# Optimization experiments

Measured on AMD Instinct MI355X. Metric: run time of the kernel, lower is better.

The kernel has to match this reference:

```python
import jax, jax.numpy as jnp
import numpy as np

N_TIME = 512          # n_time_nodes
LATENT = 32           # latent_dim
HIDDEN = 64           # hidden_dim
N_MODES = 8           # r_fourier_modes
X_A0 = 0.3            # initial stoichiometry (anode)
CSANMAX = 28700.0     # max concentration scale
BASE_LOGIT = float(np.log(X_A0 / (1.0 - X_A0)))  # logit_from_fraction(x_a0)
FEAT_DIM = 1 + 2 * N_MODES   # [rho, cos(k*pi*rho), sin(k*pi*rho)]
IN_DIM = LATENT + FEAT_DIM
N_POINTS = 2_000_000


def setup_inputs() -> dict:
    key = jax.random.key(0)
    ks = jax.random.split(key, 8)
    time_idx = jax.random.randint(ks[0], (N_POINTS,), 0, N_TIME)
    rho = jax.random.uniform(ks[1], (N_POINTS,), dtype=jnp.float32)
    # trainable latent code per nonzero time node
    emb = jax.random.normal(ks[2], (N_TIME - 1, LATENT), dtype=jnp.float32) * 0.02
    # decoder_a: Linear(IN,HID)+SiLU, Linear(HID,HID)+SiLU, Linear(HID,1)
    W0 = jax.random.normal(ks[3], (IN_DIM, HIDDEN), dtype=jnp.float32) / np.sqrt(IN_DIM)
    b0 = jnp.zeros((HIDDEN,), jnp.float32)
    W1 = jax.random.normal(ks[4], (HIDDEN, HIDDEN), dtype=jnp.float32) / np.sqrt(HIDDEN)
    b1 = jnp.zeros((HIDDEN,), jnp.float32)
    Wout = jax.random.normal(ks[5], (HIDDEN, 1), dtype=jnp.float32) * 0.1
    bout = jnp.zeros((1,), jnp.float32)
    return {"time_idx": time_idx, "rho": rho, "emb": emb,
            "W0": W0, "b0": b0, "W1": W1, "b1": b1, "Wout": Wout, "bout": bout}


def _radius_features(rho):
    # [N] -> [N, 1 + 2*N_MODES]
    k = jnp.arange(1, N_MODES + 1, dtype=rho.dtype)
    ang = jnp.pi * rho[:, None] * k[None, :]
    return jnp.concatenate([rho[:, None], jnp.cos(ang), jnp.sin(ang)], axis=1)


def reference(time_idx, rho, emb, W0, b0, W1, b1, Wout, bout):
    # predicated version of the torch masked scatter: compute everywhere,
    # select initial-condition value where time_idx == 0
    idx = jnp.clip(time_idx - 1, 0, N_TIME - 2)       # safe gather index
    e = emb[idx]                                       # [N, LATENT]
    feat = _radius_features(rho)                       # [N, FEAT_DIM]
    h = jnp.concatenate([e, feat], axis=1)             # [N, IN_DIM]
    h = jax.nn.silu(h @ W0 + b0)
    h = jax.nn.silu(h @ W1 + b1)
    raw = (h @ Wout + bout)[:, 0]                      # [N]
    theta = jax.nn.sigmoid(raw + BASE_LOGIT)
    return jnp.where(time_idx == 0, X_A0 * CSANMAX, theta * CSANMAX)
```

## Files before the change

kernel.cpp:

```cpp
#include <hip/hip_runtime.h>
#include <stdint.h>


typedef _Float16 half8  __attribute__((ext_vector_type(8)));
typedef _Float16 half4v __attribute__((ext_vector_type(4)));
typedef _Float16 half2v __attribute__((ext_vector_type(2)));
typedef float f32x4 __attribute__((ext_vector_type(4)));

#define LOG2E 1.44269504088896340736f
#define BASE_LOGIT -0.84729786038720367f
#define CSANMAX 28700.0f
#define IC_VAL 8610.0f

__device__ __forceinline__ float fast_exp2(float x) { return __builtin_amdgcn_exp2f(x); }
__device__ __forceinline__ float fast_rcp(float x)  { return __builtin_amdgcn_rcpf(x); }
__device__ __forceinline__ float sigf(float x)  { return fast_rcp(1.0f + fast_exp2(-LOG2E * x)); }
__device__ __forceinline__ void silu2(float x0, float x1, float& y0, float& y1) {
  const float d0 = 1.0f + fast_exp2(-LOG2E * x0);
  const float d1 = 1.0f + fast_exp2(-LOG2E * x1);
  const float r  = fast_rcp(d0 * d1);
  y0 = x0 * d1 * r;
  y1 = x1 * d0 * r;
}
__device__ __forceinline__ half2v pkh(float a, float b) {
  return __builtin_bit_cast(half2v, __builtin_amdgcn_cvt_pkrtz(a, b));
}

union H8 { half8 v8; half2v v2[4]; };
union H4 { half4v v4; half2v v2[2]; };

template <int CTRL>
__device__ __forceinline__ float dpp_radd(float x) {
  int yi = __builtin_amdgcn_update_dpp(0, __builtin_bit_cast(int, x), CTRL, 0xF, 0xF, false);
  return x + __builtin_bit_cast(float, yi);
}
__device__ __forceinline__ float row_sum16(float x) {
  x = dpp_radd<0xB1>(x);
  x = dpp_radd<0x4E>(x);
  x = dpp_radd<0x141>(x);
  x = dpp_radd<0x140>(x);
  return x;
}

__global__ __launch_bounds__(256) void mlp_kernel(
    const int* __restrict__ tix, const float* __restrict__ rho,
    const float* __restrict__ emb, const float* __restrict__ W0,
    const float* __restrict__ b0, const float* __restrict__ W1,
    const float* __restrict__ b1, const float* __restrict__ Wout,
    const float* __restrict__ bout, float* __restrict__ out, int ngroups)
{
  __shared__ __align__(16) _Float16 Wlds0[2][4][64][8];
  __shared__ __align__(16) _Float16 Wlds1[2][4][64][8];
  __shared__ __align__(16) _Float16 ldsH[4][16][72];

  const int tid  = threadIdx.x;
  const int wid  = tid >> 6;
  const int lane = tid & 63;
  const int m    = lane & 15;
  const int q    = lane >> 4;

  _Float16 (*Hb)[72] = ldsH[wid];

  if (wid == 0) {
#pragma unroll
    for (int t = 0; t < 4; ++t) {
#pragma unroll
      for (int s = 0; s < 2; ++s) {
        half8 f0, f1;
#pragma unroll
        for (int j = 0; j < 8; ++j) {
          const int k = s * 32 + q * 8 + j;
          const int n = t * 16 + m;
          float v0;
          if (k < 32) {
            v0 = W0[k * 64 + n];
          } else {
            const int kn = k - 32;
            v0 = (kn < 16) ? W0[(33 + kn) * 64 + n]
               : (kn == 16) ? W0[32 * 64 + n]
               : (kn == 17) ? b0[n] : 0.0f;
          }
          f0[j] = (_Float16)v0;
          f1[j] = (_Float16)W1[k * 64 + n];
        }
        *(half8*)&Wlds0[s][t][lane][0] = f0;
        *(half8*)&Wlds1[s][t][lane][0] = f1;
      }
    }
  }

  float b1n[4], woutm[4];
#pragma unroll
  for (int t = 0; t < 4; ++t) {
    b1n[t]   = b1[t * 16 + m];
    woutm[t] = Wout[t * 16 + m];
  }
  const float boutBL = bout[0] + BASE_LOGIT;

  __syncthreads();

  const f32x4 z = {0.0f, 0.0f, 0.0f, 0.0f};
  const int gstride = gridDim.x * 4;

  int g = blockIdx.x * 4 + wid;
  if (g >= ngroups) return;

  int   tiL = tix[g * 64 + lane];
  float rh  = rho[g * 64 + lane];

  for (; g < ngroups; g += gstride) {
    const int gbase = g * 64;

    const int gn = (g + gstride < ngroups) ? (g + gstride) : g;
    const int   tiLn = tix[gn * 64 + lane];
    const float rhn  = rho[gn * 64 + lane];

    float dcar = 0.0f;

#pragma unroll
    for (int st = 0; st < 4; ++st) {
      const int tim  = __shfl(tiL, st * 16 + m, 64);
      const int idxm = min(max(tim - 1, 0), 510);
      const float* erow = emb + (size_t)idxm * 32 + q * 8;
      const f32x4 e0 = *(const f32x4*)erow;
      const f32x4 e1 = *(const f32x4*)(erow + 4);

      const float rhp = __shfl(rh, st * 16 + m, 64);
      const float rev = 0.5f * rhp;
      const float c1  = __builtin_amdgcn_cosf(rev);
      const float s1f = __builtin_amdgcn_sinf(rev);
      const float tc  = 2.0f * c1;
      const float x1v = (q == 0) ? c1 : s1f;
      const float x0v = (q == 0) ? 1.0f : 0.0f;
      const float x2v = tc * x1v - x0v;
      const float x3v = tc * x2v - x1v;
      const float x4v = tc * x3v - x2v;
      const float x5v = tc * x4v - x3v;
      const float x6v = tc * x5v - x4v;
      const float x7v = tc * x6v - x5v;
      const float x8v = tc * x7v - x6v;
      H8 X1;
      X1.v2[0] = pkh(x1v, x2v);
      X1.v2[1] = pkh(x3v, x4v);
      X1.v2[2] = pkh(x5v, x6v);
      X1.v2[3] = pkh(x7v, x8v);
      {
        const half2v z2 = {};
        const half2v pr = pkh(rhp, 1.0f);
        const bool hi = (q >= 2);
        X1.v2[0] = hi ? ((q == 2) ? pr : z2) : X1.v2[0];
        X1.v2[1] = hi ? z2 : X1.v2[1];
        X1.v2[2] = hi ? z2 : X1.v2[2];
        X1.v2[3] = hi ? z2 : X1.v2[3];
      }
      H8 X0;
      X0.v2[0] = pkh(e0[0], e0[1]); X0.v2[1] = pkh(e0[2], e0[3]);
      X0.v2[2] = pkh(e1[0], e1[1]); X0.v2[3] = pkh(e1[2], e1[3]);

      f32x4 acc[4];
#pragma unroll
      for (int t = 0; t < 4; ++t) {
        const half8 wA = *(const half8*)&Wlds0[0][t][lane][0];
        const half8 wB = *(const half8*)&Wlds0[1][t][lane][0];
        f32x4 a = __builtin_amdgcn_mfma_f32_16x16x32_f16(wA, X0.v8, z, 0, 0, 0);
        a = __builtin_amdgcn_mfma_f32_16x16x32_f16(wB, X1.v8, a, 0, 0, 0);
        acc[t] = a;
      }
#pragma unroll
      for (int t = 0; t < 4; ++t) {
        float s0, s1v, s2, s3;
        silu2(acc[t][0], acc[t][1], s0, s1v);
        silu2(acc[t][2], acc[t][3], s2, s3);
        H4 hh;
        hh.v2[0] = pkh(s0, s1v);
        hh.v2[1] = pkh(s2, s3);
        *(half4v*)&Hb[m][t * 16 + q * 4] = hh.v4;
      }

      const half8 Y0 = *(const half8*)&Hb[m][q * 8];
      const half8 Y1 = *(const half8*)&Hb[m][32 + q * 8];
#pragma unroll
      for (int t = 0; t < 4; ++t) {
        const half8 w1A = *(const half8*)&Wlds1[0][t][lane][0];
        const half8 w1B = *(const half8*)&Wlds1[1][t][lane][0];
        const f32x4 binit = {b1n[t], b1n[t], b1n[t], b1n[t]};
        f32x4 a = __builtin_amdgcn_mfma_f32_16x16x32_f16(Y0, w1A, binit, 0, 0, 0);
        a = __builtin_amdgcn_mfma_f32_16x16x32_f16(Y1, w1B, a, 0, 0, 0);
        acc[t] = a;
      }
      float dot0 = 0.0f, dot1 = 0.0f, dot2 = 0.0f, dot3 = 0.0f;
#pragma unroll
      for (int t = 0; t < 4; ++t) {
        float s0, s1v, s2, s3;
        silu2(acc[t][0], acc[t][1], s0, s1v);
        silu2(acc[t][2], acc[t][3], s2, s3);
        dot0 = fmaf(s0,  woutm[t], dot0);
        dot1 = fmaf(s1v, woutm[t], dot1);
        dot2 = fmaf(s2,  woutm[t], dot2);
        dot3 = fmaf(s3,  woutm[t], dot3);
      }
      dot0 = row_sum16(dot0);
      dot1 = row_sum16(dot1);
      dot2 = row_sum16(dot2);
      dot3 = row_sum16(dot3);
      const float dsel = (m & 2) ? ((m & 1) ? dot3 : dot2) : ((m & 1) ? dot1 : dot0);
      const float dg = __shfl(dsel, (m >> 2) * 16 + (m & 3), 64);
      dcar = (q == st) ? dg : dcar;
    }

    const float theta = sigf(dcar + boutBL);
    out[gbase + lane] = (tiL == 0) ? IC_VAL : theta * CSANMAX;

    tiL = tiLn; rh = rhn;
  }
}

extern "C" void kernel_launch(void* const* d_in, const int* in_sizes, int n_in,
                              void* d_out, int out_size, void* d_ws, size_t ws_size,
                              hipStream_t stream) {
  const int*   tix  = (const int*)d_in[0];
  const float* rho  = (const float*)d_in[1];
  const float* emb  = (const float*)d_in[2];
  const float* W0   = (const float*)d_in[3];
  const float* b0   = (const float*)d_in[4];
  const float* W1   = (const float*)d_in[5];
  const float* b1   = (const float*)d_in[6];
  const float* Wout = (const float*)d_in[7];
  const float* bout = (const float*)d_in[8];
  float* outp = (float*)d_out;

  const int n       = in_sizes[0];
  const int ngroups = n / 64;

  int grid = 1536;
  const int maxg = (ngroups + 3) / 4;
  if (grid > maxg) grid = maxg;
  mlp_kernel<<<dim3(grid), dim3(256), 0, stream>>>(
      tix, rho, emb, W0, b0, W1, b1, Wout, bout, outp, ngroups);
}
```

Before: 174.8 us.

## Process two 16-point subtiles together to interleave independent MFMA chains

```diff
diff --git a/kernel.cpp b/kernel.cpp
--- a/kernel.cpp
+++ b/kernel.cpp
@@ -51,15 +51,13 @@
 {
   __shared__ __align__(16) _Float16 Wlds0[2][4][64][8];
   __shared__ __align__(16) _Float16 Wlds1[2][4][64][8];
-  __shared__ __align__(16) _Float16 ldsH[4][16][72];
+  __shared__ __align__(16) _Float16 ldsH[4][2][16][72];
 
   const int tid  = threadIdx.x;
   const int wid  = tid >> 6;
   const int lane = tid & 63;
   const int m    = lane & 15;
   const int q    = lane >> 4;
-
-  _Float16 (*Hb)[72] = ldsH[wid];
 
   if (wid == 0) {
 #pragma unroll
@@ -118,94 +116,133 @@
     float dcar = 0.0f;
 
 #pragma unroll
-    for (int st = 0; st < 4; ++st) {
-      const int tim  = __shfl(tiL, st * 16 + m, 64);
-      const int idxm = min(max(tim - 1, 0), 510);
-      const float* erow = emb + (size_t)idxm * 32 + q * 8;
-      const f32x4 e0 = *(const f32x4*)erow;
-      const f32x4 e1 = *(const f32x4*)(erow + 4);
-
-      const float rhp = __shfl(rh, st * 16 + m, 64);
-      const float rev = 0.5f * rhp;
-      const float c1  = __builtin_amdgcn_cosf(rev);
-      const float s1f = __builtin_amdgcn_sinf(rev);
-      const float tc  = 2.0f * c1;
-      const float x1v = (q == 0) ? c1 : s1f;
-      const float x0v = (q == 0) ? 1.0f : 0.0f;
-      const float x2v = tc * x1v - x0v;
-      const float x3v = tc * x2v - x1v;
-      const float x4v = tc * x3v - x2v;
-      const float x5v = tc * x4v - x3v;
-      const float x6v = tc * x5v - x4v;
-      const float x7v = tc * x6v - x5v;
-      const float x8v = tc * x7v - x6v;
-      H8 X1;
-      X1.v2[0] = pkh(x1v, x2v);
-      X1.v2[1] = pkh(x3v, x4v);
-      X1.v2[2] = pkh(x5v, x6v);
-      X1.v2[3] = pkh(x7v, x8v);
-      {
+    for (int p = 0; p < 2; ++p) {
+      const int st0 = 2 * p, st1 = 2 * p + 1;
+      _Float16 (*Hb0)[72] = ldsH[wid][0];
+      _Float16 (*Hb1)[72] = ldsH[wid][1];
+
+      half8 w0A[4], w0B[4];
+#pragma unroll
+      for (int t = 0; t < 4; ++t) {
+        w0A[t] = *(const half8*)&Wlds0[0][t][lane][0];
+        w0B[t] = *(const half8*)&Wlds0[1][t][lane][0];
+      }
+
+      const int tim0 = __shfl(tiL, st0 * 16 + m, 64);
+      const int tim1 = __shfl(tiL, st1 * 16 + m, 64);
+      const float* er0 = emb + (size_t)min(max(tim0 - 1, 0), 510) * 32 + q * 8;
+      const float* er1 = emb + (size_t)min(max(tim1 - 1, 0), 510) * 32 + q * 8;
+      const f32x4 e00 = *(const f32x4*)er0;
+      const f32x4 e01 = *(const f32x4*)(er0 + 4);
+      const f32x4 e10 = *(const f32x4*)er1;
+      const f32x4 e11 = *(const f32x4*)(er1 + 4);
+
+      H8 X1a, X1b;
+#pragma unroll
+      for (int u = 0; u < 2; ++u) {
+        const int stu = 2 * p + u;
+        const float rhp = __shfl(rh, stu * 16 + m, 64);
+        const float rev = 0.5f * rhp;
+        const float c1  = __builtin_amdgcn_cosf(rev);
+        const float s1f = __builtin_amdgcn_sinf(rev);
+        const float tc  = 2.0f * c1;
+        const float x1v = (q == 0) ? c1 : s1f;
+        const float x0v = (q == 0) ? 1.0f : 0.0f;
+        const float x2v = tc * x1v - x0v;
+        const float x3v = tc * x2v - x1v;
+        const float x4v = tc * x3v - x2v;
+        const float x5v = tc * x4v - x3v;
+        const float x6v = tc * x5v - x4v;
+        const float x7v = tc * x6v - x5v;
+        const float x8v = tc * x7v - x6v;
+        H8 X;
+        X.v2[0] = pkh(x1v, x2v);
+        X.v2[1] = pkh(x3v, x4v);
+        X.v2[2] = pkh(x5v, x6v);
+        X.v2[3] = pkh(x7v, x8v);
         const half2v z2 = {};
         const half2v pr = pkh(rhp, 1.0f);
         const bool hi = (q >= 2);
-        X1.v2[0] = hi ? ((q == 2) ? pr : z2) : X1.v2[0];
-        X1.v2[1] = hi ? z2 : X1.v2[1];
-        X1.v2[2] = hi ? z2 : X1.v2[2];
-        X1.v2[3] = hi ? z2 : X1.v2[3];
-      }
-      H8 X0;
-      X0.v2[0] = pkh(e0[0], e0[1]); X0.v2[1] = pkh(e0[2], e0[3]);
-      X0.v2[2] = pkh(e1[0], e1[1]); X0.v2[3] = pkh(e1[2], e1[3]);
-
-      f32x4 acc[4];
-#pragma unroll
-      for (int t = 0; t < 4; ++t) {
-        const half8 wA = *(const half8*)&Wlds0[0][t][lane][0];
-        const half8 wB = *(const half8*)&Wlds0[1][t][lane][0];
-        f32x4 a = __builtin_amdgcn_mfma_f32_16x16x32_f16(wA, X0.v8, z, 0, 0, 0);
-        a = __builtin_amdgcn_mfma_f32_16x16x32_f16(wB, X1.v8, a, 0, 0, 0);
-        acc[t] = a;
+        X.v2[0] = hi ? ((q == 2) ? pr : z2) : X.v2[0];
+        X.v2[1] = hi ? z2 : X.v2[1];
+        X.v2[2] = hi ? z2 : X.v2[2];
+        X.v2[3] = hi ? z2 : X.v2[3];
+        if (u == 0) X1a = X; else X1b = X;
+      }
+      H8 X0a, X0b;
+      X0a.v2[0] = pkh(e00[0], e00[1]); X0a.v2[1] = pkh(e00[2], e00[3]);
+      X0a.v2[2] = pkh(e01[0], e01[1]); X0a.v2[3] = pkh(e01[2], e01[3]);
+      X0b.v2[0] = pkh(e10[0], e10[1]); X0b.v2[1] = pkh(e10[2], e10[3]);
+      X0b.v2[2] = pkh(e11[0], e11[1]); X0b.v2[3] = pkh(e11[2], e11[3]);
+
+      f32x4 accA[4], accB[4];
+#pragma unroll
+      for (int t = 0; t < 4; ++t) {
+        f32x4 a = __builtin_amdgcn_mfma_f32_16x16x32_f16(w0A[t], X0a.v8, z, 0, 0, 0);
+        accA[t] = __builtin_amdgcn_mfma_f32_16x16x32_f16(w0B[t], X1a.v8, a, 0, 0, 0);
+        f32x4 b = __builtin_amdgcn_mfma_f32_16x16x32_f16(w0A[t], X0b.v8, z, 0, 0, 0);
+        accB[t] = __builtin_amdgcn_mfma_f32_16x16x32_f16(w0B[t], X1b.v8, b, 0, 0, 0);
       }
 #pragma unroll
       for (int t = 0; t < 4; ++t) {
         float s0, s1v, s2, s3;
-        silu2(acc[t][0], acc[t][1], s0, s1v);
-        silu2(acc[t][2], acc[t][3], s2, s3);
-        H4 hh;
-        hh.v2[0] = pkh(s0, s1v);
-        hh.v2[1] = pkh(s2, s3);
-        *(half4v*)&Hb[m][t * 16 + q * 4] = hh.v4;
-      }
-
-      const half8 Y0 = *(const half8*)&Hb[m][q * 8];
-      const half8 Y1 = *(const half8*)&Hb[m][32 + q * 8];
-#pragma unroll
-      for (int t = 0; t < 4; ++t) {
-        const half8 w1A = *(const half8*)&Wlds1[0][t][lane][0];
-        const half8 w1B = *(const half8*)&Wlds1[1][t][lane][0];
+        silu2(accA[t][0], accA[t][1], s0, s1v);
+        silu2(accA[t][2], accA[t][3], s2, s3);
+        H4 hh; hh.v2[0] = pkh(s0, s1v); hh.v2[1] = pkh(s2, s3);
+        *(half4v*)&Hb0[m][t * 16 + q * 4] = hh.v4;
+      }
+#pragma unroll
+      for (int t = 0; t < 4; ++t) {
+        float s0, s1v, s2, s3;
+        silu2(accB[t][0], accB[t][1], s0, s1v);
+        silu2(accB[t][2], accB[t][3], s2, s3);
+        H4 hh; hh.v2[0] = pkh(s0, s1v); hh.v2[1] = pkh(s2, s3);
+        *(half4v*)&Hb1[m][t * 16 + q * 4] = hh.v4;
+      }
+
+      half8 w1A[4], w1B[4];
+#pragma unroll
+      for (int t = 0; t < 4; ++t) {
+        w1A[t] = *(const half8*)&Wlds1[0][t][lane][0];
+        w1B[t] = *(const half8*)&Wlds1[1][t][lane][0];
+      }
+      const half8 Y0a = *(const half8*)&Hb0[m][q * 8];
+      const half8 Y1a = *(const half8*)&Hb0[m][32 + q * 8];
+      const half8 Y0b = *(const half8*)&Hb1[m][q * 8];
+      const half8 Y1b = *(const half8*)&Hb1[m][32 + q * 8];
+
+#pragma unroll
+      for (int t = 0; t < 4; ++t) {
         const f32x4 binit = {b1n[t], b1n[t], b1n[t], b1n[t]};
-        f32x4 a = __builtin_amdgcn_mfma_f32_16x16x32_f16(Y0, w1A, binit, 0, 0, 0);
-        a = __builtin_amdgcn_mfma_f32_16x16x32_f16(Y1, w1B, a, 0, 0, 0);
-        acc[t] = a;
-      }
-      float dot0 = 0.0f, dot1 = 0.0f, dot2 = 0.0f, dot3 = 0.0f;
-#pragma unroll
-      for (int t = 0; t < 4; ++t) {
-        float s0, s1v, s2, s3;
-        silu2(acc[t][0], acc[t][1], s0, s1v);
-        silu2(acc[t][2], acc[t][3], s2, s3);
-        dot0 = fmaf(s0,  woutm[t], dot0);
-        dot1 = fmaf(s1v, woutm[t], dot1);
-        dot2 = fmaf(s2,  woutm[t], dot2);
-        dot3 = fmaf(s3,  woutm[t], dot3);
-      }
-      dot0 = row_sum16(dot0);
-      dot1 = row_sum16(dot1);
-      dot2 = row_sum16(dot2);
-      dot3 = row_sum16(dot3);
-      const float dsel = (m & 2) ? ((m & 1) ? dot3 : dot2) : ((m & 1) ? dot1 : dot0);
-      const float dg = __shfl(dsel, (m >> 2) * 16 + (m & 3), 64);
-      dcar = (q == st) ? dg : dcar;
+        f32x4 a = __builtin_amdgcn_mfma_f32_16x16x32_f16(Y0a, w1A[t], binit, 0, 0, 0);
+        accA[t] = __builtin_amdgcn_mfma_f32_16x16x32_f16(Y1a, w1B[t], a, 0, 0, 0);
+        f32x4 b = __builtin_amdgcn_mfma_f32_16x16x32_f16(Y0b, w1A[t], binit, 0, 0, 0);
+        accB[t] = __builtin_amdgcn_mfma_f32_16x16x32_f16(Y1b, w1B[t], b, 0, 0, 0);
+      }
+
+#pragma unroll
+      for (int u = 0; u < 2; ++u) {
+        const f32x4* acc = (u == 0) ? accA : accB;
+        const int stu = 2 * p + u;
+        float dot0 = 0.0f, dot1 = 0.0f, dot2 = 0.0f, dot3 = 0.0f;
+#pragma unroll
+        for (int t = 0; t < 4; ++t) {
+          float s0, s1v, s2, s3;
+          silu2(acc[t][0], acc[t][1], s0, s1v);
+          silu2(acc[t][2], acc[t][3], s2, s3);
+          dot0 = fmaf(s0,  woutm[t], dot0);
+          dot1 = fmaf(s1v, woutm[t], dot1);
+          dot2 = fmaf(s2,  woutm[t], dot2);
+          dot3 = fmaf(s3,  woutm[t], dot3);
+        }
+        dot0 = row_sum16(dot0);
+        dot1 = row_sum16(dot1);
+        dot2 = row_sum16(dot2);
+        dot3 = row_sum16(dot3);
+        const float dsel = (m & 2) ? ((m & 1) ? dot3 : dot2) : ((m & 1) ? dot1 : dot0);
+        const float dg = __shfl(dsel, (m >> 2) * 16 + (m & 3), 64);
+        dcar = (q == stu) ? dg : dcar;
+      }
     }
 
     const float theta = sigf(dcar + boutBL);
@@ -232,7 +269,7 @@
   const int n       = in_sizes[0];
   const int ngroups = n / 64;
 
-  int grid = 1536;
+  int grid = 1024;
   const int maxg = (ngroups + 3) / 4;
   if (grid > maxg) grid = maxg;
   mlp_kernel<<<dim3(grid), dim3(256), 0, stream>>>(
```

After: 176.8 us. No clear change (+1.1%).
